# Performance work log

Hardware: AMD Instinct MI355X
Metric: run time of the kernel (lower is better)

Reference implementation:

```python
import jax, jax.numpy as jnp
import numpy as np

EPS = 1e-8
ALPHA = 0.3
PATTERN_W = 0.1


def setup_inputs() -> dict:
    key = jax.random.key(0)
    ks = jax.random.split(key, 6)
    H, W, D, Hid = 1024, 1024, 32, 64
    return {
        "grid_states": jax.random.normal(ks[0], (H, W, D), dtype=jnp.float32),
        "potentials": jax.random.uniform(ks[1], (H, W), dtype=jnp.float32),
        "W1": jax.random.normal(ks[2], (D + 1, Hid), dtype=jnp.float32) * 0.1,
        "b1": jax.random.normal(ks[3], (Hid,), dtype=jnp.float32) * 0.1,
        "W2": jax.random.normal(ks[4], (Hid, D), dtype=jnp.float32) * 0.1,
        "b2": jax.random.normal(ks[5], (D,), dtype=jnp.float32) * 0.1,
    }


def reference(grid_states, potentials, W1, b1, W2, b2):
    # self_similarity: A^3 normalized to unit length, rescaled by ||A||
    cube = grid_states * grid_states * grid_states                     # [H,W,D]
    cube_norm = jnp.linalg.norm(cube, axis=-1, keepdims=True)          # [H,W,1]
    cell_norm = jnp.linalg.norm(grid_states, axis=-1, keepdims=True)   # [H,W,1]
    self_pattern = cube / (cube_norm + EPS) * cell_norm                # [H,W,D]

    cell_with_pattern = grid_states + PATTERN_W * self_pattern         # [H,W,D]

    # transform_net on [cell_with_pattern ; potential]
    x = jnp.concatenate([cell_with_pattern, potentials[..., None]], axis=-1)  # [H,W,D+1]
    h = jax.nn.relu(jnp.einsum("hwc,cf->hwf", x, W1) + b1)             # [H,W,Hid]
    transformed = jnp.einsum("hwf,fd->hwd", h, W2) + b2                # [H,W,D]

    # new_state = transform + alpha * cell  (neighbor influence path only
    # affects role_value, which forward() discards)
    return transformed + ALPHA * grid_states
```

## Files before the change

### kernel.cpp

```cpp
#include <hip/hip_runtime.h>

#define DIM   32
#define HID   64

typedef __attribute__((ext_vector_type(8))) short bf16x8;
typedef __attribute__((ext_vector_type(4))) float f32x4;

__device__ __forceinline__ unsigned cvt_pk_bf16(float lo, float hi) {
    unsigned r;
    asm("v_cvt_pk_bf16_f32 %0, %1, %2" : "=v"(r) : "v"(lo), "v"(hi));
    return r;
}
__device__ __forceinline__ float bfp_lo(unsigned u) { return __uint_as_float(u << 16); }
__device__ __forceinline__ float bfp_hi(unsigned u) { return __uint_as_float(u & 0xFFFF0000u); }

__device__ __forceinline__ void plswap(unsigned &a, unsigned &b) {
    auto r = __builtin_amdgcn_permlane32_swap((int)a, (int)b, false, false);
    a = (unsigned)r[0];
    b = (unsigned)r[1];
}

struct f2 { float a, b; };
__device__ __forceinline__ f2 plswap16v(float a, float b) {
    auto r = __builtin_amdgcn_permlane16_swap(__float_as_int(a), __float_as_int(b),
                                              false, false);
    return { __int_as_float(r[0]), __int_as_float(r[1]) };
}

__device__ __forceinline__ float quad_sum(float x) {
    auto r1 = __builtin_amdgcn_permlane32_swap(__float_as_int(x), __float_as_int(x),
                                               false, false);
    float t = __int_as_float(r1[0]) + __int_as_float(r1[1]);
    auto r2 = __builtin_amdgcn_permlane16_swap(__float_as_int(t), __float_as_int(t),
                                               false, false);
    return __int_as_float(r2[0]) + __int_as_float(r2[1]);
}

union bfu { bf16x8 v; unsigned u[4]; };

__global__ __launch_bounds__(64, 3) void behavior_mfma(
    const float* __restrict__ g_in,
    const float* __restrict__ pot,
    const float* __restrict__ W1,
    const float* __restrict__ b1,
    const float* __restrict__ W2,
    const float* __restrict__ b2,
    float* __restrict__ out)
{
    const int lane = threadIdx.x & 63;
    const int quad = lane >> 4;
    const int mrow = lane & 15;

    const long cell0 = (long)blockIdx.x * 128;

    float4 gA[2][2], gB[2][2]; float pV[2][2];
    auto loadPair = [&](int s, long cb) {
        #pragma unroll
        for (int u = 0; u < 2; ++u) {
            const float* gp = g_in + (cb + u * 16 + mrow) * DIM + quad * 8;
            gA[s][u] = ((const float4*)gp)[0];
            gB[s][u] = ((const float4*)gp)[1];
            pV[s][u] = pot[cb + u * 16 + mrow];
        }
    };
    loadPair(0, cell0);
    loadPair(1, cell0 + 32);

    bf16x8 w1f[4];
    #pragma unroll
    for (int nb = 0; nb < 4; ++nb) {
        bfu t;
        #pragma unroll
        for (int jp = 0; jp < 4; ++jp)
            t.u[jp] = cvt_pk_bf16(W1[(quad * 8 + 2 * jp)     * HID + nb * 16 + mrow],
                                  W1[(quad * 8 + 2 * jp + 1) * HID + nb * 16 + mrow]);
        w1f[nb] = t.v;
    }
    bf16x8 w2f[2][2];
    #pragma unroll
    for (int kc = 0; kc < 2; ++kc)
        #pragma unroll
        for (int nc = 0; nc < 2; ++nc) {
            bfu t;
            #pragma unroll
            for (int jp = 0; jp < 4; ++jp) {
                const int j0 = 2 * jp;
                const int r0 = kc * 32 + (quad >> 1) * 16 + (quad & 1) * 4
                             + ((j0 >> 2) << 3) + (j0 & 3);
                t.u[jp] = cvt_pk_bf16(W2[r0 * DIM + nc * 16 + mrow],
                                      W2[(r0 + 1) * DIM + nc * 16 + mrow]);
            }
            w2f[kc][nc] = t.v;
        }
    bf16x8 aid[2];
    #pragma unroll
    for (int nc = 0; nc < 2; ++nc) {
        bfu t;
        #pragma unroll
        for (int jp = 0; jp < 4; ++jp) {
            unsigned lo = (quad * 8 + 2 * jp     == nc * 16 + mrow) ? 0x00003F80u : 0u;
            unsigned hi = (quad * 8 + 2 * jp + 1 == nc * 16 + mrow) ? 0x3F800000u : 0u;
            t.u[jp] = lo | hi;
        }
        aid[nc] = t.v;
    }
    unsigned w1pp[4][2], b1p[4][2];
    #pragma unroll
    for (int nb = 0; nb < 4; ++nb)
        #pragma unroll
        for (int p = 0; p < 2; ++p) {
            w1pp[nb][p] = cvt_pk_bf16(W1[32 * HID + nb * 16 + quad * 4 + 2 * p],
                                      W1[32 * HID + nb * 16 + quad * 4 + 2 * p + 1]);
            b1p[nb][p]  = cvt_pk_bf16(b1[nb * 16 + quad * 4 + 2 * p],
                                      b1[nb * 16 + quad * 4 + 2 * p + 1]);
        }
    unsigned b2p[2][2];
    #pragma unroll
    for (int nc = 0; nc < 2; ++nc)
        #pragma unroll
        for (int p = 0; p < 2; ++p)
            b2p[nc][p] = cvt_pk_bf16(b2[nc * 16 + quad * 4 + 2 * p],
                                     b2[nc * 16 + quad * 4 + 2 * p + 1]);

    auto stageA = [&](float4 a, float4 b, float potv, bfu& h0, bfu& h1, bfu& gf) {
        float gv[8] = {a.x, a.y, a.z, a.w, b.x, b.y, b.z, b.w};
        float cube[8];
        float tp = 0.f, sp = 0.f;
        #pragma unroll
        for (int j = 0; j < 8; ++j) {
            float gc = gv[j];
            float g2 = gc * gc;
            float g3 = g2 * gc;
            tp += g2;
            sp = fmaf(g3, g3, sp);
            cube[j] = g3;
        }
        tp = quad_sum(tp);
        sp = quad_sum(sp);
        const float scale = 0.1f * __builtin_amdgcn_sqrtf(tp) *
                            __builtin_amdgcn_rcpf(__builtin_amdgcn_sqrtf(sp) + 1e-8f);

        bfu xf;
        #pragma unroll
        for (int jp = 0; jp < 4; ++jp) {
            xf.u[jp] = cvt_pk_bf16(fmaf(scale, cube[2 * jp],     gv[2 * jp]),
                                   fmaf(scale, cube[2 * jp + 1], gv[2 * jp + 1]));
            gf.u[jp] = cvt_pk_bf16(0.3f * gv[2 * jp], 0.3f * gv[2 * jp + 1]);
        }

        unsigned P[4][2];
        #pragma unroll
        for (int nb = 0; nb < 4; ++nb) {
            f32x4 c1;
            c1[0] = fmaf(potv, bfp_lo(w1pp[nb][0]), bfp_lo(b1p[nb][0]));
            c1[1] = fmaf(potv, bfp_hi(w1pp[nb][0]), bfp_hi(b1p[nb][0]));
            c1[2] = fmaf(potv, bfp_lo(w1pp[nb][1]), bfp_lo(b1p[nb][1]));
            c1[3] = fmaf(potv, bfp_hi(w1pp[nb][1]), bfp_hi(b1p[nb][1]));
            c1 = __builtin_amdgcn_mfma_f32_16x16x32_bf16(w1f[nb], xf.v, c1, 0, 0, 0);
            P[nb][0] = cvt_pk_bf16(fmaxf(c1[0], 0.f), fmaxf(c1[1], 0.f));
            P[nb][1] = cvt_pk_bf16(fmaxf(c1[2], 0.f), fmaxf(c1[3], 0.f));
        }

        {
            unsigned x0 = P[0][0], y0 = P[1][0]; plswap(x0, y0);
            unsigned x1 = P[0][1], y1 = P[1][1]; plswap(x1, y1);
            h0.u[0] = x0; h0.u[1] = x1; h0.u[2] = y0; h0.u[3] = y1;
        }
        {
            unsigned x0 = P[2][0], y0 = P[3][0]; plswap(x0, y0);
            unsigned x1 = P[2][1], y1 = P[3][1]; plswap(x1, y1);
            h1.u[0] = x0; h1.u[1] = x1; h1.u[2] = y0; h1.u[3] = y1;
        }
    };

    auto gemm2st = [&](const bfu& h0, const bfu& h1, const bfu& gf, long cb) {
        f32x4 A, B;
        #pragma unroll
        for (int nc = 0; nc < 2; ++nc) {
            f32x4 c2;
            c2[0] = bfp_lo(b2p[nc][0]);
            c2[1] = bfp_hi(b2p[nc][0]);
            c2[2] = bfp_lo(b2p[nc][1]);
            c2[3] = bfp_hi(b2p[nc][1]);
            c2 = __builtin_amdgcn_mfma_f32_16x16x32_bf16(aid[nc],    gf.v, c2, 0, 0, 0);
            c2 = __builtin_amdgcn_mfma_f32_16x16x32_bf16(w2f[0][nc], h0.v, c2, 0, 0, 0);
            c2 = __builtin_amdgcn_mfma_f32_16x16x32_bf16(w2f[1][nc], h1.v, c2, 0, 0, 0);
            if (nc == 0) A = c2; else B = c2;
        }
        #pragma unroll
        for (int r = 0; r < 4; ++r) {
            float ar = A[r], br = B[r];
            f2 sw = plswap16v(ar, br);
            A[r] = sw.a; B[r] = sw.b;
        }
        const int colq = ((quad & 1) << 4) | ((quad >> 1) << 3);
        float* op = out + (cb + mrow) * DIM + colq;
        *(f32x4*)op       = A;
        *(f32x4*)(op + 4) = B;
    };

    #pragma unroll
    for (int it = 0; it < 4; ++it) {
        const int s = it & 1;
        const float4 a0 = gA[s][0], b0 = gB[s][0]; const float p0 = pV[s][0];
        const float4 a1 = gA[s][1], b1x = gB[s][1]; const float p1 = pV[s][1];
        if (it + 2 < 4) loadPair(s, cell0 + (long)(it + 2) * 32);

        bfu h00, h01, g0, h10, h11, g1;
        stageA(a0, b0,  p0, h00, h01, g0);
        stageA(a1, b1x, p1, h10, h11, g1);

        const long cb = cell0 + (long)it * 32;
        gemm2st(h00, h01, g0, cb);
        gemm2st(h10, h11, g1, cb + 16);
    }
}

extern "C" void kernel_launch(void* const* d_in, const int* in_sizes, int n_in,
                              void* d_out, int out_size, void* d_ws, size_t ws_size,
                              hipStream_t stream) {
    const float* g_in = (const float*)d_in[0];
    const float* pot  = (const float*)d_in[1];
    const float* W1   = (const float*)d_in[2];
    const float* b1   = (const float*)d_in[3];
    const float* W2   = (const float*)d_in[4];
    const float* b2   = (const float*)d_in[5];
    float* out = (float*)d_out;

    const int n_cells = in_sizes[1];
    const int cells_per_block = 128;
    const int blocks = (n_cells + cells_per_block - 1) / cells_per_block;

    behavior_mfma<<<blocks, 64, 0, stream>>>(g_in, pot, W1, b1, W2, b2, out);
}
```

Measured before the change: 245.8 us.

## Stage grid and potential tiles into LDS via async global_load_lds

Instead of register double-buffering two 32-cell pairs, the kernel issues every tile's grid-state and potential loads for the block up front. They go straight into LDS through global_load_lds, then a plain loop reads each 16-cell tile from LDS after an s_waitcnt. The aim is more loads in flight per wave and less VGPR pressure from prefetch buffers. The trade-off is about 17 KB of LDS per block, which can limit occupancy. The fixed vmcnt(14) wait inside a rolled loop relies on how the compiler orders the surrounding weight loads and output stores, so it is fragile.

Result: no change. 247.8 us (+0.8%).

```diff
diff --git a/kernel.cpp b/kernel.cpp
--- a/kernel.cpp
+++ b/kernel.cpp
@@ -2,6 +2,7 @@
 
 #define DIM   32
 #define HID   64
+#define TILES 8
 
 typedef __attribute__((ext_vector_type(8))) short bf16x8;
 typedef __attribute__((ext_vector_type(4))) float f32x4;
@@ -36,7 +37,20 @@
     return __int_as_float(r2[0]) + __int_as_float(r2[1]);
 }
 
+typedef const __attribute__((address_space(1))) void gas_t;
+typedef __attribute__((address_space(3))) void las_t;
+__device__ __forceinline__ void stage16(const void* g, void* l) {
+    __builtin_amdgcn_global_load_lds((gas_t*)g, (las_t*)l, 16, 0, 0);
+}
+__device__ __forceinline__ void stage4(const void* g, void* l) {
+    __builtin_amdgcn_global_load_lds((gas_t*)g, (las_t*)l, 4, 0, 0);
+}
+
 union bfu { bf16x8 v; unsigned u[4]; };
+
+#define SG_A   0
+#define SG_B   8192
+#define SG_P   16384
 
 __global__ __launch_bounds__(64, 3) void behavior_mfma(
     const float* __restrict__ g_in,
@@ -47,24 +61,25 @@
     const float* __restrict__ b2,
     float* __restrict__ out)
 {
+    __shared__ __align__(16) char sStage[16896];
+
     const int lane = threadIdx.x & 63;
     const int quad = lane >> 4;
     const int mrow = lane & 15;
 
-    const long cell0 = (long)blockIdx.x * 128;
-
-    float4 gA[2][2], gB[2][2]; float pV[2][2];
-    auto loadPair = [&](int s, long cb) {
-        #pragma unroll
-        for (int u = 0; u < 2; ++u) {
-            const float* gp = g_in + (cb + u * 16 + mrow) * DIM + quad * 8;
-            gA[s][u] = ((const float4*)gp)[0];
-            gB[s][u] = ((const float4*)gp)[1];
-            pV[s][u] = pot[cb + u * 16 + mrow];
-        }
-    };
-    loadPair(0, cell0);
-    loadPair(1, cell0 + 32);
+    const long cell0 = (long)blockIdx.x * (TILES * 16);
+
+    stage4(pot + cell0 + lane,        sStage + SG_P);
+    stage4(pot + cell0 + 64 + lane,   sStage + SG_P + 256);
+    {
+        const float* gb = g_in + cell0 * DIM;
+        #pragma unroll
+        for (int t = 0; t < TILES; ++t) {
+            const float* gp = gb + (t * 16 + mrow) * DIM + quad * 8;
+            stage16(gp,     sStage + SG_A + t * 1024);
+            stage16(gp + 4, sStage + SG_B + t * 1024);
+        }
+    }
 
     bf16x8 w1f[4];
     #pragma unroll
@@ -199,20 +214,15 @@
         *(f32x4*)(op + 4) = B;
     };
 
-    #pragma unroll
-    for (int it = 0; it < 4; ++it) {
-        const int s = it & 1;
-        const float4 a0 = gA[s][0], b0 = gB[s][0]; const float p0 = pV[s][0];
-        const float4 a1 = gA[s][1], b1x = gB[s][1]; const float p1 = pV[s][1];
-        if (it + 2 < 4) loadPair(s, cell0 + (long)(it + 2) * 32);
-
-        bfu h00, h01, g0, h10, h11, g1;
-        stageA(a0, b0,  p0, h00, h01, g0);
-        stageA(a1, b1x, p1, h10, h11, g1);
-
-        const long cb = cell0 + (long)it * 32;
-        gemm2st(h00, h01, g0, cb);
-        gemm2st(h10, h11, g1, cb + 16);
+    for (int t = 0; t < TILES; ++t) {
+        asm volatile("s_waitcnt vmcnt(14)" ::: "memory");
+        const float4 a    = *(const float4*)(sStage + SG_A + t * 1024 + lane * 16);
+        const float4 b    = *(const float4*)(sStage + SG_B + t * 1024 + lane * 16);
+        const float  potv = *(const float*) (sStage + SG_P + (t * 16 + mrow) * 4);
+
+        bfu h0, h1, gf;
+        stageA(a, b, potv, h0, h1, gf);
+        gemm2st(h0, h1, gf, cell0 + (long)t * 16);
     }
 }
 
@@ -228,7 +238,7 @@
     float* out = (float*)d_out;
 
     const int n_cells = in_sizes[1];
-    const int cells_per_block = 128;
+    const int cells_per_block = TILES * 16;
     const int blocks = (n_cells + cells_per_block - 1) / cells_per_block;
 
     behavior_mfma<<<blocks, 64, 0, stream>>>(g_in, pot, W1, b1, W2, b2, out);
```
